# Performance work log

Measured on AMD Instinct MI355X. Metric: run time of the kernel, lower is better.

## Reference

```python
import jax, jax.numpy as jnp
import numpy as np

UPSCALER = 4

def setup_inputs() -> dict:
    key = jax.random.key(0)
    x = jax.random.normal(key, (8, 256, 16384), dtype=jnp.float32)
    return {"x": x}

def reference(x) -> jnp.ndarray:
    # PixelShuffle1d: out[b, c', l*u + j] = x[b, c'*u + j, l]
    b, c, l = x.shape
    u = UPSCALER
    # (B, C, L) -> (B, C//u, u, L) -> (B, C//u, L, u) -> (B, C//u, L*u)
    y = x.reshape(b, c // u, u, l)
    y = jnp.transpose(y, (0, 1, 3, 2))
    return y.reshape(b, c // u, l * u)
```

## Files before the change

### kernel.cpp

```cpp
#include <hip/hip_runtime.h>


constexpr int L = 16384;
constexpr long TOTAL_QUADS = 8L * 64L * 16384L;

__global__ __launch_bounds__(256) void pixel_shuffle1d_kernel(
    const float* __restrict__ x, float* __restrict__ out) {
    long tid = (long)blockIdx.x * blockDim.x + threadIdx.x;
    if (tid >= TOTAL_QUADS) return;

    int l  = (int)(tid & (L - 1));
    long bc = tid >> 14;

    const float* src = x + bc * (4L * L) + l;
    float4 v;
    v.x = src[0L * L];
    v.y = src[1L * L];
    v.z = src[2L * L];
    v.w = src[3L * L];

    reinterpret_cast<float4*>(out)[tid] = v;
}

extern "C" void kernel_launch(void* const* d_in, const int* in_sizes, int n_in,
                              void* d_out, int out_size, void* d_ws, size_t ws_size,
                              hipStream_t stream) {
    const float* x = (const float*)d_in[0];
    float* out = (float*)d_out;

    const int block = 256;
    const long grid = (TOTAL_QUADS + block - 1) / block;
    pixel_shuffle1d_kernel<<<(int)grid, block, 0, stream>>>(x, out);
}
```

Measured before the change: 218.2 us.

## Stage rows through LDS tiles to use vectorized float4 global loads

Each block now loads a 1024-element tile from the four source channel rows using float4 loads into shared memory, synchronizes, then reassembles interleaved float4 outputs from LDS. This replaces four scalar strided loads per thread with wide vector loads, cutting memory instruction count. It adds an LDS round trip and a barrier per block, and each block does more work.

```diff
diff --git a/kernel.cpp b/kernel.cpp
--- a/kernel.cpp
+++ b/kernel.cpp
@@ -2,24 +2,35 @@
 
 
 constexpr int L = 16384;
-constexpr long TOTAL_QUADS = 8L * 64L * 16384L;
+constexpr int TILE_L = 1024;
+constexpr int TILES_PER_ROW = L / TILE_L;
+constexpr int BLOCK = 256;
+constexpr int QPR = L / 4;
 
 __global__ __launch_bounds__(256) void pixel_shuffle1d_kernel(
     const float* __restrict__ x, float* __restrict__ out) {
-    long tid = (long)blockIdx.x * blockDim.x + threadIdx.x;
-    if (tid >= TOTAL_QUADS) return;
+    __shared__ float lds[4][TILE_L];
 
-    int l  = (int)(tid & (L - 1));
-    long bc = tid >> 14;
+    const int t = threadIdx.x;
+    const int tile = blockIdx.x & (TILES_PER_ROW - 1);
+    const long bc = blockIdx.x >> 4;
+    const int l0 = tile * TILE_L;
 
-    const float* src = x + bc * (4L * L) + l;
-    float4 v;
-    v.x = src[0L * L];
-    v.y = src[1L * L];
-    v.z = src[2L * L];
-    v.w = src[3L * L];
+    const float4* src = reinterpret_cast<const float4*>(x + bc * (4L * L) + l0);
+#pragma unroll
+    for (int r = 0; r < 4; ++r) {
+        float4 v = src[r * QPR + t];
+        *reinterpret_cast<float4*>(&lds[r][t * 4]) = v;
+    }
 
-    reinterpret_cast<float4*>(out)[tid] = v;
+    __syncthreads();
+
+    float4* dst = reinterpret_cast<float4*>(out) + (bc << 14) + l0;
+#pragma unroll
+    for (int i = 0; i < 4; ++i) {
+        int k = i * BLOCK + t;
+        dst[k] = make_float4(lds[0][k], lds[1][k], lds[2][k], lds[3][k]);
+    }
 }
 
 extern "C" void kernel_launch(void* const* d_in, const int* in_sizes, int n_in,
@@ -28,7 +39,6 @@
     const float* x = (const float*)d_in[0];
     float* out = (float*)d_out;
 
-    const int block = 256;
-    const long grid = (TOTAL_QUADS + block - 1) / block;
-    pixel_shuffle1d_kernel<<<(int)grid, block, 0, stream>>>(x, out);
+    const int grid = (8 * 64) * TILES_PER_ROW;
+    pixel_shuffle1d_kernel<<<grid, BLOCK, 0, stream>>>(x, out);
 }
```

Measured after the change: 227.1 us. +4.1%, slower.
